# Performance work log

Hardware: AMD Instinct MI355X
Metric: run time of the kernel (lower is better)

Reference implementation:

```python
import jax, jax.numpy as jnp
import numpy as np

N_IN = 100000   # active voxels at coarse level
N_OUT = 400000  # active voxels at fine level
K = 8           # 2x2x2 kernel offsets of the inverse conv
P = 100000      # rulebook pairs per kernel offset
C_IN, C_OUT, C_SKIP = 128, 64, 64
EPS = 1e-5


def setup_inputs() -> dict:
    key = jax.random.key(0)
    k1, k2, k3, k4, k5, k6 = jax.random.split(key, 6)
    x_feats = jax.random.normal(k1, (N_IN, C_IN), jnp.float32)
    skip_feats = jax.random.normal(k2, (N_OUT, C_SKIP), jnp.float32)
    W_deconv = jax.random.normal(k3, (K, C_IN, C_OUT), jnp.float32) * (1.0 / np.sqrt(C_IN * K))
    gamma = jnp.ones((C_OUT,), jnp.float32)
    beta = jnp.zeros((C_OUT,), jnp.float32)
    W_fuse = jax.random.normal(k4, (C_OUT + C_SKIP, C_OUT), jnp.float32) * (1.0 / np.sqrt(C_OUT + C_SKIP))
    in_idx = jax.random.randint(k5, (K, P), 0, N_IN, jnp.int32)
    out_idx = jax.random.randint(k6, (K, P), 0, N_OUT, jnp.int32)
    return {"x_feats": x_feats, "skip_feats": skip_feats, "W_deconv": W_deconv,
            "gamma": gamma, "beta": beta, "W_fuse": W_fuse,
            "in_idx": in_idx, "out_idx": out_idx}


def reference(x_feats, skip_feats, W_deconv, gamma, beta, W_fuse, in_idx, out_idx):
    # --- SparseInverseConv3d: gather-GEMM-scatter over the rulebook ---
    gathered = x_feats[in_idx]                                  # [K,P,C_IN]
    contrib = jnp.einsum('kpi,kio->kpo', gathered, W_deconv)    # [K,P,C_OUT]
    y = jnp.zeros((N_OUT, C_OUT), x_feats.dtype)
    y = y.at[out_idx.reshape(-1)].add(contrib.reshape(-1, C_OUT))
    # --- BatchNorm1d (batch stats, biased var) + ReLU on voxel features ---
    mean = jnp.mean(y, axis=0)
    var = jnp.mean((y - mean) ** 2, axis=0)
    y = (y - mean) * jax.lax.rsqrt(var + EPS) * gamma + beta
    y = jax.nn.relu(y)
    # --- channel concat with skip, then SubMConv3d(kernel=1) == linear ---
    z = jnp.concatenate([y, skip_feats], axis=1)                # [N_OUT, C_OUT+C_SKIP]
    return z @ W_fuse                                           # [N_OUT, C_OUT]
```

## Files before the change

kernel.cpp:

```cpp
#include <hip/hip_runtime.h>

#define N_IN   100000
#define N_OUT  400000
#define KK     8
#define PP     100000
#define C_IN   128
#define C_OUTC 64
#define C_SKIP 64
#define EPS_BN 1e-5f
#define SLOTS  16

typedef __attribute__((ext_vector_type(8))) short bf16x8;
typedef __attribute__((ext_vector_type(4))) float f32x4;

__device__ __forceinline__ unsigned short f2b(float f) {
    unsigned int u = __builtin_bit_cast(unsigned int, f);
    return (unsigned short)((u + 0x7FFFu + ((u >> 16) & 1u)) >> 16);
}
__device__ __forceinline__ float b2f(unsigned short v) {
    return __builtin_bit_cast(float, (unsigned)v << 16);
}

__global__ __launch_bounds__(256) void prep_all(
    const float4* __restrict__ x, const float* __restrict__ Wd,
    unsigned short* __restrict__ xb, unsigned short* __restrict__ bfrag,
    int4* __restrict__ counts4, float4* __restrict__ mid4)
{
    const int t = blockIdx.x * 256 + threadIdx.x;
    if (t < N_IN * C_IN / 8) {
        const float4 v0 = x[2 * t], v1 = x[2 * t + 1];
        uint4 o;
        o.x = f2b(v0.x) | ((unsigned)f2b(v0.y) << 16);
        o.y = f2b(v0.z) | ((unsigned)f2b(v0.w) << 16);
        o.z = f2b(v1.x) | ((unsigned)f2b(v1.y) << 16);
        o.w = f2b(v1.z) | ((unsigned)f2b(v1.w) << 16);
        ((uint4*)xb)[t] = o;
    }
    if (t < N_OUT / 4)
        counts4[t] = (int4){0, 0, 0, 0};
    if (t < (32 * 128) / 4)
        mid4[t] = (float4){0.f, 0.f, 0.f, 0.f};
    if (t < KK * 4 * 4 * 64 * 8) {
        const int j  = t & 7;
        const int l  = (t >> 3) & 63;
        const int ct = (t >> 9) & 3;
        const int ks = (t >> 11) & 3;
        const int ko = t >> 13;
        const int i  = ks * 32 + (l >> 4) * 8 + j;
        const int c  = ct * 16 + (l & 15);
        bfrag[t] = f2b(Wd[((size_t)ko * C_IN + i) * C_OUTC + c]);
    }
}

__global__ __launch_bounds__(256) void gemm_fill(
    const unsigned short* __restrict__ xb, const unsigned short* __restrict__ bfrag,
    unsigned short* __restrict__ z,
    const int* __restrict__ in_idx, const int* __restrict__ out_idx,
    int* __restrict__ counts, int* __restrict__ slots)
{
    if (blockIdx.x >= N_IN / 32) {
        const int q = ((int)blockIdx.x - N_IN / 32) * 256 + (int)threadIdx.x;
        if (q < KK * PP) {
            const int row = out_idx[q];
            const int pk  = in_idx[q] * KK + q / PP;
            const int idx = atomicAdd(&counts[row], 1);
            if (idx < SLOTS) slots[(size_t)row * SLOTS + idx] = pk;
        }
        return;
    }

    __shared__ __align__(16) unsigned short alds[32 * 136];
    const int rb = blockIdx.x * 32;
    for (int cch = threadIdx.x; cch < 32 * 16; cch += 256) {
        const int row = cch >> 4, ch = cch & 15;
        *(uint4*)(&alds[row * 136 + ch * 8]) =
            *(const uint4*)(xb + (size_t)(rb + row) * C_IN + ch * 8);
    }
    __syncthreads();

    const int wv  = threadIdx.x >> 6;
    const int l   = threadIdx.x & 63;
    const int r16 = l & 15, hi = l >> 4;

    f32x4 acc[2][2][4];
    #pragma unroll
    for (int q = 0; q < 2; ++q)
        #pragma unroll
        for (int rt = 0; rt < 2; ++rt)
            #pragma unroll
            for (int ct = 0; ct < 4; ++ct)
                acc[q][rt][ct] = (f32x4){0.f, 0.f, 0.f, 0.f};

    #pragma unroll
    for (int ks = 0; ks < 4; ++ks) {
        const bf16x8 a0 = *(const bf16x8*)(&alds[r16 * 136 + ks * 32 + hi * 8]);
        const bf16x8 a1 = *(const bf16x8*)(&alds[(16 + r16) * 136 + ks * 32 + hi * 8]);
        #pragma unroll
        for (int q = 0; q < 2; ++q) {
            const unsigned short* __restrict__ bk = bfrag + (size_t)(wv * 2 + q) * 8192;
            #pragma unroll
            for (int ct = 0; ct < 4; ++ct) {
                const bf16x8 b = *(const bf16x8*)(bk + ((ks * 4 + ct) * 64 + l) * 8);
                acc[q][0][ct] = __builtin_amdgcn_mfma_f32_16x16x32_bf16(a0, b, acc[q][0][ct], 0, 0, 0);
                acc[q][1][ct] = __builtin_amdgcn_mfma_f32_16x16x32_bf16(a1, b, acc[q][1][ct], 0, 0, 0);
            }
        }
    }

    #pragma unroll
    for (int q = 0; q < 2; ++q) {
        const int k = wv * 2 + q;
        #pragma unroll
        for (int rt = 0; rt < 2; ++rt)
            #pragma unroll
            for (int ct = 0; ct < 4; ++ct)
                #pragma unroll
                for (int j = 0; j < 4; ++j)
                    z[((size_t)(rb + rt * 16 + hi * 4 + j) * KK + k) * 64 + ct * 16 + r16]
                        = f2b(acc[q][rt][ct][j]);
    }
}

__global__ __launch_bounds__(512) void gather_yb(
    const unsigned short* __restrict__ z, const int* __restrict__ counts,
    const int* __restrict__ slots, unsigned short* __restrict__ yb,
    float* __restrict__ mid)
{
    const int tid = threadIdx.x, lane = tid & 63;
    const int gw  = (int)blockIdx.x * 8 + (tid >> 6);
    const int r0  = gw * 8;

    const int4 c0 = *(const int4*)(counts + r0);
    const int4 c1 = *(const int4*)(counts + r0 + 4);
    const int cnt[8] = {c0.x, c0.y, c0.z, c0.w, c1.x, c1.y, c1.z, c1.w};
    int4 s4[8];
    #pragma unroll
    for (int i = 0; i < 8; ++i)
        s4[i] = *(const int4*)(slots + (size_t)(r0 + i) * SLOTS);

    float ssum = 0.f, ssq = 0.f;
    float a[8];
    #pragma unroll
    for (int i = 0; i < 8; ++i) {
        const int c  = cnt[i] > SLOTS ? SLOTS : cnt[i];
        const int p0 = c > 0 ? s4[i].x : 0;
        const int p1 = c > 1 ? s4[i].y : 0;
        const int p2 = c > 2 ? s4[i].z : 0;
        const int p3 = c > 3 ? s4[i].w : 0;
        const float v0 = b2f(z[(size_t)p0 * 64 + lane]);
        const float v1 = b2f(z[(size_t)p1 * 64 + lane]);
        const float v2 = b2f(z[(size_t)p2 * 64 + lane]);
        const float v3 = b2f(z[(size_t)p3 * 64 + lane]);
        float s = (c > 0 ? v0 : 0.f) + (c > 1 ? v1 : 0.f);
        s += (c > 2 ? v2 : 0.f) + (c > 3 ? v3 : 0.f);
        if (c > 4) {
            for (int j = 4; j < c; ++j)
                s += b2f(z[(size_t)slots[(size_t)(r0 + i) * SLOTS + j] * 64 + lane]);
        }
        a[i] = s;
    }
    #pragma unroll
    for (int i = 0; i < 8; ++i) {
        yb[(size_t)(r0 + i) * C_OUTC + lane] = f2b(a[i]);
        ssum += a[i];
        ssq = fmaf(a[i], a[i], ssq);
    }

    __shared__ float rs[512], rq[512];
    rs[tid] = ssum; rq[tid] = ssq;
    __syncthreads();
    if (tid < 64) {
        float s = 0.f, q2 = 0.f;
        #pragma unroll
        for (int w = 0; w < 8; ++w) { s += rs[tid + w * 64]; q2 += rq[tid + w * 64]; }
        float* mrow = mid + (size_t)(blockIdx.x & 31) * 128;
        atomicAdd(&mrow[tid], s);
        atomicAdd(&mrow[64 + tid], q2);
    }
}

__global__ void finalize_p(const float* __restrict__ mid,
                           const float* __restrict__ gamma,
                           const float* __restrict__ beta,
                           const float* __restrict__ Wf,
                           float* __restrict__ sc,
                           unsigned short* __restrict__ wf_frag)
{
    __shared__ float acc2[128];
    __shared__ float bsh[C_OUTC];
    __shared__ float ssc[C_OUTC];
    const int t = threadIdx.x;
    float s = 0.f;
    #pragma unroll
    for (int b = 0; b < 32; ++b) s += mid[(size_t)b * 128 + t];
    acc2[t] = s;
    __syncthreads();
    if (t < 64) {
        const float inv_n = 1.0f / (float)N_OUT;
        const float mean  = acc2[t] * inv_n;
        const float var   = acc2[64 + t] * inv_n - mean * mean;
        const float sg    = gamma[t] * rsqrtf(var + EPS_BN);
        const float b     = beta[t] - mean * sg;
        sc[t]            = sg;
        sc[C_OUTC + t]   = -b / sg;
        ssc[t] = sg;
        bsh[t] = b;
    }
    __syncthreads();
    if (t < 64) {
        float acc = 0.f;
        for (int i = 0; i < C_OUTC; ++i)
            acc = fmaf(bsh[i], Wf[i * C_OUTC + t], acc);
        sc[2 * C_OUTC + t] = acc;
    }
    for (int e = t; e < 4 * 4 * 64 * 8; e += 128) {
        const int j  = e & 7;
        const int l  = (e >> 3) & 63;
        const int ct = (e >> 9) & 3;
        const int ks = e >> 11;
        const int i  = ks * 32 + (l >> 4) * 8 + j;
        const int c  = ct * 16 + (l & 15);
        float w = Wf[(size_t)i * C_OUTC + c];
        if (i < C_OUTC) w *= ssc[i];
        wf_frag[e] = f2b(w);
    }
}

__global__ __launch_bounds__(256) void fuse_mfma_b(
    const unsigned short* __restrict__ yb, const float* __restrict__ skip,
    const unsigned short* __restrict__ wf_frag, const float* __restrict__ sc,
    float* __restrict__ out)
{
    __shared__ __align__(16) unsigned short alds[128 * 136];
    __shared__ float nbsh[C_OUTC];
    const int rb = blockIdx.x * 128;
    if (threadIdx.x < C_OUTC) nbsh[threadIdx.x] = sc[C_OUTC + threadIdx.x];
    __syncthreads();

    const uint4* __restrict__ yb4 = (const uint4*)(yb + (size_t)rb * C_OUTC);
    for (int e = threadIdx.x; e < 128 * 8; e += 256) {
        const int row = e >> 3, q = e & 7;
        uint4 v = yb4[row * 8 + q];
        uint4 o;
        unsigned* vp = (unsigned*)&v;
        unsigned* op = (unsigned*)&o;
        #pragma unroll
        for (int h = 0; h < 4; ++h) {
            const float lo = fmaxf(b2f((unsigned short)(vp[h] & 0xFFFF)), nbsh[q * 8 + h * 2]);
            const float hf = fmaxf(b2f((unsigned short)(vp[h] >> 16)),    nbsh[q * 8 + h * 2 + 1]);
            op[h] = f2b(lo) | ((unsigned)f2b(hf) << 16);
        }
        *(uint4*)(&alds[row * 136 + q * 8]) = o;
    }
    const float4* __restrict__ s4 = (const float4*)(skip + (size_t)rb * C_SKIP);
    for (int e = threadIdx.x; e < 128 * 16; e += 256) {
        const int row = e >> 4, q = e & 15;
        const float4 v = s4[row * 16 + q];
        uint2 p;
        p.x = f2b(v.x) | ((unsigned)f2b(v.y) << 16);
        p.y = f2b(v.z) | ((unsigned)f2b(v.w) << 16);
        *(uint2*)(&alds[row * 136 + 64 + q * 4]) = p;
    }
    __syncthreads();

    const int w   = threadIdx.x >> 6;
    const int l   = threadIdx.x & 63;
    const int r16 = l & 15, hi = l >> 4;
    const int rw  = w * 32;

    f32x4 acc[2][4];
    #pragma unroll
    for (int ct = 0; ct < 4; ++ct) {
        const float b0 = sc[2 * C_OUTC + ct * 16 + r16];
        acc[0][ct] = (f32x4){b0, b0, b0, b0};
        acc[1][ct] = (f32x4){b0, b0, b0, b0};
    }

    #pragma unroll
    for (int ks = 0; ks < 4; ++ks) {
        const bf16x8 a0 = *(const bf16x8*)(&alds[(rw + r16) * 136 + ks * 32 + hi * 8]);
        const bf16x8 a1 = *(const bf16x8*)(&alds[(rw + 16 + r16) * 136 + ks * 32 + hi * 8]);
        #pragma unroll
        for (int ct = 0; ct < 4; ++ct) {
            const bf16x8 b = *(const bf16x8*)(wf_frag + ((ks * 4 + ct) * 64 + l) * 8);
            acc[0][ct] = __builtin_amdgcn_mfma_f32_16x16x32_bf16(a0, b, acc[0][ct], 0, 0, 0);
            acc[1][ct] = __builtin_amdgcn_mfma_f32_16x16x32_bf16(a1, b, acc[1][ct], 0, 0, 0);
        }
    }

    #pragma unroll
    for (int rt = 0; rt < 2; ++rt)
        #pragma unroll
        for (int ct = 0; ct < 4; ++ct)
            #pragma unroll
            for (int j = 0; j < 4; ++j)
                out[(size_t)(rb + rw + rt * 16 + hi * 4 + j) * C_OUTC + ct * 16 + r16]
                    = acc[rt][ct][j];
}

extern "C" void kernel_launch(void* const* d_in, const int* in_sizes, int n_in,
                              void* d_out, int out_size, void* d_ws, size_t ws_size,
                              hipStream_t stream)
{
    const float* x      = (const float*)d_in[0];
    const float* skip   = (const float*)d_in[1];
    const float* Wd     = (const float*)d_in[2];
    const float* gamma  = (const float*)d_in[3];
    const float* beta   = (const float*)d_in[4];
    const float* Wf     = (const float*)d_in[5];
    const int*   in_idx  = (const int*)d_in[6];
    const int*   out_idx = (const int*)d_in[7];

    float* y  = (float*)d_out;
    float* sc = (float*)d_ws + 128;

    char* p = (char*)d_ws + 4096;
    unsigned short* xb      = (unsigned short*)p;  p += (size_t)N_IN * C_IN * 2;
    unsigned short* bfrag   = (unsigned short*)p;  p += (size_t)KK * 8192 * 2;
    unsigned short* wf_frag = (unsigned short*)p;  p += 8192 * 2;
    int*   counts   = (int*)p;                     p += (size_t)N_OUT * 4;
    int*   slots    = (int*)p;                     p += (size_t)N_OUT * SLOTS * 4;
    float* mid      = (float*)p;                   p += (size_t)32 * 128 * 4;
    unsigned short* z = (unsigned short*)p;        p += (size_t)N_IN * KK * C_OUTC * 2;
    unsigned short* yb = (unsigned short*)p;

    prep_all<<<(N_IN * C_IN / 8 + 255) / 256, 256, 0, stream>>>(
        (const float4*)x, Wd, xb, bfrag, (int4*)counts, (float4*)mid);
    gemm_fill<<<N_IN / 32 + (KK * PP + 255) / 256, 256, 0, stream>>>(
        xb, bfrag, z, in_idx, out_idx, counts, slots);
    gather_yb<<<N_OUT / 64, 512, 0, stream>>>(z, counts, slots, yb, mid);
    finalize_p<<<1, 128, 0, stream>>>(mid, gamma, beta, Wf, sc, wf_frag);
    fuse_mfma_b<<<N_OUT / 128, 256, 0, stream>>>(yb, skip, wf_frag, sc, y);
}
```

Before: 266.6 us.

## Fuse bf16 conversion of input features into GEMM tile load, split CSR fill kernel

Removes the separate pass that converts x_feats to a bf16 buffer. The GEMM kernel now reads fp32 rows directly and converts them while staging into LDS. The rulebook bucketing is split out of the merged GEMM kernel into its own launch. This saves a full write and re-read of the converted activations, at the cost of reading fp32 in the GEMM and one extra kernel launch.

```diff
diff --git a/kernel.cpp b/kernel.cpp
--- a/kernel.cpp
+++ b/kernel.cpp
@@ -22,20 +22,10 @@
 }
 
 __global__ __launch_bounds__(256) void prep_all(
-    const float4* __restrict__ x, const float* __restrict__ Wd,
-    unsigned short* __restrict__ xb, unsigned short* __restrict__ bfrag,
+    const float* __restrict__ Wd, unsigned short* __restrict__ bfrag,
     int4* __restrict__ counts4, float4* __restrict__ mid4)
 {
     const int t = blockIdx.x * 256 + threadIdx.x;
-    if (t < N_IN * C_IN / 8) {
-        const float4 v0 = x[2 * t], v1 = x[2 * t + 1];
-        uint4 o;
-        o.x = f2b(v0.x) | ((unsigned)f2b(v0.y) << 16);
-        o.y = f2b(v0.z) | ((unsigned)f2b(v0.w) << 16);
-        o.z = f2b(v1.x) | ((unsigned)f2b(v1.y) << 16);
-        o.w = f2b(v1.z) | ((unsigned)f2b(v1.w) << 16);
-        ((uint4*)xb)[t] = o;
-    }
     if (t < N_OUT / 4)
         counts4[t] = (int4){0, 0, 0, 0};
     if (t < (32 * 128) / 4)
@@ -52,29 +42,33 @@
     }
 }
 
-__global__ __launch_bounds__(256) void gemm_fill(
-    const unsigned short* __restrict__ xb, const unsigned short* __restrict__ bfrag,
-    unsigned short* __restrict__ z,
+__global__ __launch_bounds__(256) void fill_csr(
     const int* __restrict__ in_idx, const int* __restrict__ out_idx,
     int* __restrict__ counts, int* __restrict__ slots)
 {
-    if (blockIdx.x >= N_IN / 32) {
-        const int q = ((int)blockIdx.x - N_IN / 32) * 256 + (int)threadIdx.x;
-        if (q < KK * PP) {
-            const int row = out_idx[q];
-            const int pk  = in_idx[q] * KK + q / PP;
-            const int idx = atomicAdd(&counts[row], 1);
-            if (idx < SLOTS) slots[(size_t)row * SLOTS + idx] = pk;
-        }
-        return;
-    }
-
+    const int q = blockIdx.x * 256 + threadIdx.x;
+    if (q < KK * PP) {
+        const int row = out_idx[q];
+        const int pk  = in_idx[q] * KK + q / PP;
+        const int idx = atomicAdd(&counts[row], 1);
+        if (idx < SLOTS) slots[(size_t)row * SLOTS + idx] = pk;
+    }
+}
+
+__global__ __launch_bounds__(256) void gemm_all(
+    const float* __restrict__ x, const unsigned short* __restrict__ bfrag,
+    unsigned short* __restrict__ z)
+{
     __shared__ __align__(16) unsigned short alds[32 * 136];
     const int rb = blockIdx.x * 32;
-    for (int cch = threadIdx.x; cch < 32 * 16; cch += 256) {
-        const int row = cch >> 4, ch = cch & 15;
-        *(uint4*)(&alds[row * 136 + ch * 8]) =
-            *(const uint4*)(xb + (size_t)(rb + row) * C_IN + ch * 8);
+    const float4* __restrict__ x4 = (const float4*)(x + (size_t)rb * C_IN);
+    for (int e = threadIdx.x; e < 32 * 32; e += 256) {
+        const int row = e >> 5, q = e & 31;
+        const float4 v = x4[row * 32 + q];
+        uint2 p;
+        p.x = f2b(v.x) | ((unsigned)f2b(v.y) << 16);
+        p.y = f2b(v.z) | ((unsigned)f2b(v.w) << 16);
+        *(uint2*)(&alds[row * 136 + q * 4]) = p;
     }
     __syncthreads();
 
@@ -315,7 +309,6 @@
     float* sc = (float*)d_ws + 128;
 
     char* p = (char*)d_ws + 4096;
-    unsigned short* xb      = (unsigned short*)p;  p += (size_t)N_IN * C_IN * 2;
     unsigned short* bfrag   = (unsigned short*)p;  p += (size_t)KK * 8192 * 2;
     unsigned short* wf_frag = (unsigned short*)p;  p += 8192 * 2;
     int*   counts   = (int*)p;                     p += (size_t)N_OUT * 4;
@@ -324,10 +317,10 @@
     unsigned short* z = (unsigned short*)p;        p += (size_t)N_IN * KK * C_OUTC * 2;
     unsigned short* yb = (unsigned short*)p;
 
-    prep_all<<<(N_IN * C_IN / 8 + 255) / 256, 256, 0, stream>>>(
-        (const float4*)x, Wd, xb, bfrag, (int4*)counts, (float4*)mid);
-    gemm_fill<<<N_IN / 32 + (KK * PP + 255) / 256, 256, 0, stream>>>(
-        xb, bfrag, z, in_idx, out_idx, counts, slots);
+    prep_all<<<(N_OUT / 4 + 255) / 256, 256, 0, stream>>>(
+        Wd, bfrag, (int4*)counts, (float4*)mid);
+    fill_csr<<<(KK * PP + 255) / 256, 256, 0, stream>>>(in_idx, out_idx, counts, slots);
+    gemm_all<<<N_IN / 32, 256, 0, stream>>>(x, bfrag, z);
     gather_yb<<<N_OUT / 64, 512, 0, stream>>>(z, counts, slots, yb, mid);
     finalize_p<<<1, 128, 0, stream>>>(mid, gamma, beta, Wf, sc, wf_frag);
     fuse_mfma_b<<<N_OUT / 128, 256, 0, stream>>>(yb, skip, wf_frag, sc, y);
```

New measurement: 269.3 us. Within noise of the previous version (+1.0%).
